# Kernel tuning notes

Hardware: AMD Instinct MI355X
Metric: run time of the kernel (lower is better)

Reference implementation:

```python
import jax, jax.numpy as jnp
import numpy as np

B, N, C, H = 8, 512, 64, 128
T, K = 10, 2                       # dilation threshold and skip divisor
TAUS = (0.25, 0.5, 0.75)
WTS = (0.25, 0.5, 0.25)
EPS_GIN = 0.0                      # (1 + eps) * x, eps buffer
AVG_DEG = 32.0


def setup_inputs() -> dict:
    key = jax.random.key(0)
    ks = jax.random.split(key, 6)
    x = jax.random.normal(ks[0], (B, N, C), jnp.float32)
    u = jax.random.uniform(ks[1], (B, N, N))
    a = u < (AVG_DEG / N)
    adj = jnp.maximum(a, jnp.swapaxes(a, 1, 2)).astype(jnp.float32)  # symmetric binary adjacency
    mask = jax.random.bernoulli(ks[2], 0.9, (B, N))
    W1 = jax.random.normal(ks[3], (C, H), jnp.float32) / np.float32(np.sqrt(C))
    b1 = jnp.zeros((H,), jnp.float32)
    W2 = jax.random.normal(ks[4], (H, C), jnp.float32) / np.float32(np.sqrt(H))
    b2 = jnp.zeros((C,), jnp.float32)
    return {"x": x, "adj": adj, "mask": mask, "W1": W1, "b1": b1, "W2": W2, "b2": b2}


def reference(x, adj, mask, W1, b1, W2, b2):
    Bc, Nc, Cc = x.shape
    eye = jnp.eye(Nc, dtype=bool)
    adj_ = jnp.where(eye, 1.0, adj)                 # add_loop=True: force self loops
    # ---- vectorized dilation (replaces the per-(b,n) python loop) ----
    neigh = (adj_ > 0) & (~eye)                     # neighbors excluding self [B,N,N]
    ni = neigh.astype(jnp.int32)
    rank = jnp.cumsum(ni, axis=-1) - ni             # exclusive rank of m among n's sorted neighbors
    nb = ni.sum(-1)                                 # [B,N] neighbor count (w/o self)
    skip = jnp.where(nb > T, (nb + K - 1) // K, 1)  # ceil(nb/k) if nb > T else 1 (linear mode, layer 1)
    skip = jnp.maximum(skip, 1)
    sk = skip[:, :, None]
    # remove relative indices skip-1, 2*skip-1, ... when skip > 1, only for masked-in nodes
    rem = neigh & (sk > 1) & ((rank % sk) == (sk - 1)) & mask[:, :, None]
    rem = rem | jnp.swapaxes(rem, 1, 2)             # symmetric removal
    adj_d = jnp.where(rem, 0.0, adj_)
    # ---- masked quantile aggregation over neighbors (== nanquantile) ----
    nd = adj_d > 0                                  # includes self loop -> at least 1 valid
    vals = jnp.where(nd[..., None], x[:, None, :, :], jnp.inf)  # [B,N,M,C]; invalid -> +inf
    s = jnp.sort(vals, axis=2)                      # valid values first, ascending
    nv = nd.sum(2)                                  # [B,N] valid count per node
    agg = jnp.zeros_like(x)
    for tau, w in zip(TAUS, WTS):                   # small fixed loop over quantiles
        pos = jnp.asarray(tau, x.dtype) * jnp.maximum(nv - 1, 0).astype(x.dtype)
        lo = jnp.floor(pos).astype(jnp.int32)
        hi = jnp.ceil(pos).astype(jnp.int32)
        frac = (pos - lo.astype(x.dtype))[..., None]
        idx_lo = jnp.broadcast_to(lo[:, :, None, None], (Bc, Nc, 1, Cc))
        idx_hi = jnp.broadcast_to(hi[:, :, None, None], (Bc, Nc, 1, Cc))
        v_lo = jnp.take_along_axis(s, idx_lo, axis=2)[:, :, 0, :]
        v_hi = jnp.take_along_axis(s, idx_hi, axis=2)[:, :, 0, :]
        agg = agg + jnp.asarray(w, x.dtype) * (v_lo + frac * (v_hi - v_lo))
    agg = jnp.where(nv[..., None] > 0, agg, 0.0)    # nan_to_num for empty rows
    out = (1.0 + EPS_GIN) * x + agg
    h = jax.nn.relu(out @ W1 + b1)                  # GIN MLP: Linear-ReLU-Linear
    y = h @ W2 + b2
    return y * mask[..., None].astype(y.dtype)
```

## Files before the change

### kernel.cpp

```cpp
#include <hip/hip_runtime.h>
#include <cstdint>

#define B_ 8
#define N_ 512
#define C_ 64
#define H_ 128
#define T_ 10
#define K_ 2
#define WPR 16
#define NVMAX 96
#define TT 8

__device__ inline uint32_t fkey(float v) {
    uint32_t bits = __float_as_uint(v);
    return (bits & 0x80000000u) ? ~bits : (bits | 0x80000000u);
}
__device__ inline float fdec(uint32_t key) {
    uint32_t ok = (key & 0xFFFFFF00u) | 0x80u;
    uint32_t bits = (ok & 0x80000000u) ? (ok ^ 0x80000000u) : ~ok;
    return __uint_as_float(bits);
}

__global__ __launch_bounds__(256) void pass1_rem(const float* __restrict__ adj,
                                                 const int* __restrict__ mask,
                                                 uint32_t* __restrict__ rembits) {
    int wid = threadIdx.x >> 6, lane = threadIdx.x & 63;
    int row = blockIdx.x * 4 + wid;
    int i = row & (N_ - 1);
    const float4* arow4 = (const float4*)(adj + (size_t)row * N_);
    float4 a0 = arow4[lane * 2];
    float4 a1 = arow4[lane * 2 + 1];
    float av[8] = {a0.x, a0.y, a0.z, a0.w, a1.x, a1.y, a1.z, a1.w};

    int flags = 0, cnt = 0;
    int jbase = lane * 8;
#pragma unroll
    for (int k = 0; k < 8; ++k) {
        int j = jbase + k;
        bool ng = (j != i) && (av[k] > 0.0f);
        flags |= ((int)ng) << k;
        cnt += (int)ng;
    }
    int inc = cnt;
#pragma unroll
    for (int d = 1; d < 64; d <<= 1) {
        int o = __shfl_up(inc, d, 64);
        if (lane >= d) inc += o;
    }
    int excl = inc - cnt;
    int nb = __shfl(inc, 63, 64);
    int skip = (nb > T_) ? ((nb + K_ - 1) / K_) : 1;
    if (skip < 1) skip = 1;
    int maski = mask[row];

    unsigned byteval = 0;
    if (skip > 1 && maski != 0) {
        int r = excl;
#pragma unroll
        for (int k = 0; k < 8; ++k) {
            if ((flags >> k) & 1) {
                if (r % skip == skip - 1) byteval |= 1u << k;
                ++r;
            }
        }
    }
    unsigned b0 = __shfl((int)byteval, (lane & 15) * 4 + 0, 64);
    unsigned b1 = __shfl((int)byteval, (lane & 15) * 4 + 1, 64);
    unsigned b2 = __shfl((int)byteval, (lane & 15) * 4 + 2, 64);
    unsigned b3 = __shfl((int)byteval, (lane & 15) * 4 + 3, 64);
    if (lane < WPR) {
        uint32_t w = b0 | (b1 << 8) | (b2 << 16) | (b3 << 24);
        rembits[(size_t)row * WPR + lane] = w;
    }
}

__global__ __launch_bounds__(256) void pass2_quant_mlp(
        const float* __restrict__ x, const float* __restrict__ adj,
        const int* __restrict__ mask, const uint32_t* __restrict__ rembits,
        const float* __restrict__ W1, const float* __restrict__ b1,
        const float* __restrict__ W2, const float* __restrict__ b2,
        float* __restrict__ out) {
    int row = blockIdx.x;
    int b = row >> 9, i = row & (N_ - 1);
    int tid = threadIdx.x;
    int lane = tid & 63;
    int q = tid >> 6;

    __shared__ unsigned short kept[NVMAX];
    __shared__ int s_cnt;
    __shared__ uint32_t keys[NVMAX * C_];
    __shared__ float selv[6][C_];
    __shared__ int s_rr[6];
    __shared__ float s_frac[3];
    __shared__ float out_node[C_];
    __shared__ float hbuf[H_];

    if (tid == 0) s_cnt = 0;
    __syncthreads();

    const float* arow = adj + (size_t)row * N_;
    const uint32_t* rrow = rembits + (size_t)row * WPR;
    const uint32_t* rbase = rembits + (size_t)(b * N_) * WPR;

    for (int jb = 0; jb < N_; jb += 256) {
        int j = jb + tid;
        bool keep;
        if (j == i) {
            keep = true;
        } else {
            keep = (arow[j] > 0.0f);
            if (keep) {
                unsigned rij = (rrow[j >> 5] >> (j & 31)) & 1u;
                unsigned rji = (rbase[(size_t)j * WPR + (i >> 5)] >> (i & 31)) & 1u;
                keep = ((rij | rji) == 0u);
            }
        }
        unsigned long long bal = __ballot(keep);
        int base = 0;
        if (lane == 0 && bal) base = atomicAdd(&s_cnt, __popcll(bal));
        base = __shfl(base, 0, 64);
        if (keep) {
            int pos = __popcll(bal & ((1ull << lane) - 1ull));
            int p = base + pos;
            if (p < NVMAX) kept[p] = (unsigned short)j;
        }
    }
    __syncthreads();
    int nv = s_cnt;
    if (nv > NVMAX) nv = NVMAX;

    const float* xb = x + (size_t)b * N_ * C_;

    for (int t = q; t < nv; t += 4) {
        float v = xb[(size_t)kept[t] * C_ + lane];
        keys[t * C_ + lane] = (fkey(v) & 0xFFFFFF00u) | (uint32_t)t;
    }

    if (tid == 0) {
        const float taus[3] = {0.25f, 0.5f, 0.75f};
        float nm1 = (float)((nv - 1 > 0) ? nv - 1 : 0);
        for (int qq = 0; qq < 3; ++qq) {
            float pos = taus[qq] * nm1;
            int lo = (int)floorf(pos);
            int hi = (int)ceilf(pos);
            s_rr[2 * qq] = lo; s_rr[2 * qq + 1] = hi;
            s_frac[qq] = pos - (float)lo;
        }
    }
    __syncthreads();

    int rr0 = s_rr[0], rr1 = s_rr[1], rr2 = s_rr[2],
        rr3 = s_rr[3], rr4 = s_rr[4], rr5 = s_rr[5];

    const uint32_t* kcol = keys + lane;

    for (int base = 0; base < nv; base += 32) {
        int tbase = base + q * TT;
        if (tbase >= nv) continue;
        uint32_t k[TT];
        int rs_a[TT], rs_b[TT];
#pragma unroll
        for (int m = 0; m < TT; ++m) {
            int t = tbase + m;
            k[m] = (t < nv) ? kcol[t * C_] : 0xFFFFFFFFu;
            rs_a[m] = 0; rs_b[m] = 0;
        }
        int u = 0;
#pragma unroll 2
        for (; u + 1 < nv; u += 2) {
            uint32_t w0 = kcol[u * C_];
            uint32_t w1 = kcol[(u + 1) * C_];
#pragma unroll
            for (int m = 0; m < TT; ++m) {
                rs_a[m] += (int)(w0 < k[m]);
                rs_b[m] += (int)(w1 < k[m]);
            }
        }
        if (u < nv) {
            uint32_t w0 = kcol[u * C_];
#pragma unroll
            for (int m = 0; m < TT; ++m) rs_a[m] += (int)(w0 < k[m]);
        }
#pragma unroll
        for (int m = 0; m < TT; ++m) {
            int rs = rs_a[m] + rs_b[m];
            bool h0 = rs == rr0, h1 = rs == rr1, h2 = rs == rr2;
            bool h3 = rs == rr3, h4 = rs == rr4, h5 = rs == rr5;
            if (h0 | h1 | h2 | h3 | h4 | h5) {
                float fv = fdec(k[m]);
                if (h0) selv[0][lane] = fv;
                if (h1) selv[1][lane] = fv;
                if (h2) selv[2][lane] = fv;
                if (h3) selv[3][lane] = fv;
                if (h4) selv[4][lane] = fv;
                if (h5) selv[5][lane] = fv;
            }
        }
    }
    __syncthreads();

    if (tid < C_) {
        float f0 = s_frac[0], f1 = s_frac[1], f2 = s_frac[2];
        float agg = 0.25f * (selv[0][tid] + f0 * (selv[1][tid] - selv[0][tid]));
        agg      += 0.5f  * (selv[2][tid] + f1 * (selv[3][tid] - selv[2][tid]));
        agg      += 0.25f * (selv[4][tid] + f2 * (selv[5][tid] - selv[4][tid]));
        out_node[tid] = xb[(size_t)i * C_ + tid] + agg;
    }
    __syncthreads();

    float maskf = (mask[row] != 0) ? 1.0f : 0.0f;
    if (tid < H_) {
        float acc = b1[tid];
        for (int c = 0; c < C_; ++c) acc += out_node[c] * W1[c * H_ + tid];
        hbuf[tid] = acc > 0.0f ? acc : 0.0f;
    }
    __syncthreads();
    if (tid < C_) {
        float acc = b2[tid];
        for (int k = 0; k < H_; ++k) acc += hbuf[k] * W2[k * C_ + tid];
        out[(size_t)row * C_ + tid] = acc * maskf;
    }
}

extern "C" void kernel_launch(void* const* d_in, const int* in_sizes, int n_in,
                              void* d_out, int out_size, void* d_ws, size_t ws_size,
                              hipStream_t stream) {
    const float* x   = (const float*)d_in[0];
    const float* adj = (const float*)d_in[1];
    const int*  mask = (const int*)d_in[2];
    const float* W1  = (const float*)d_in[3];
    const float* b1  = (const float*)d_in[4];
    const float* W2  = (const float*)d_in[5];
    const float* b2  = (const float*)d_in[6];
    float* out = (float*)d_out;

    uint32_t* rembits = (uint32_t*)d_ws;

    hipLaunchKernelGGL(pass1_rem, dim3(B_ * N_ / 4), dim3(256), 0, stream,
                       adj, mask, rembits);
    hipLaunchKernelGGL(pass2_quant_mlp, dim3(B_ * N_), dim3(256), 0, stream,
                       x, adj, mask, rembits, W1, b1, W2, b2, out);
}
```

Measured before the change: 165.2 us.

## Precompute keep bitmask in pass1 and transpose sort keys into uint4 columns

Pass1 now writes a per-row keep bitmask (adjacency plus self loop minus removed edges), so pass2 reads only bitmasks and no longer touches the dense float adjacency row. The rank-counting keys move to a transposed, padded uint4 layout, so each lane reads four keys per LDS access instead of one strided word. The padded stride of 25 is meant to avoid bank conflicts. Padding to a multiple of four with sentinel keys makes the count loop branch-free. The cost is that keep symmetry now depends on looking up the transposed bit in the other row.

```diff
diff --git a/kernel.cpp b/kernel.cpp
--- a/kernel.cpp
+++ b/kernel.cpp
@@ -10,6 +10,7 @@
 #define WPR 16
 #define NVMAX 96
 #define TT 8
+#define KS4 25
 
 __device__ inline uint32_t fkey(float v) {
     uint32_t bits = __float_as_uint(v);
@@ -21,9 +22,9 @@
     return __uint_as_float(bits);
 }
 
-__global__ __launch_bounds__(256) void pass1_rem(const float* __restrict__ adj,
-                                                 const int* __restrict__ mask,
-                                                 uint32_t* __restrict__ rembits) {
+__global__ __launch_bounds__(256) void pass1_keep(const float* __restrict__ adj,
+                                                  const int* __restrict__ mask,
+                                                  uint32_t* __restrict__ keepbits) {
     int wid = threadIdx.x >> 6, lane = threadIdx.x & 63;
     int row = blockIdx.x * 4 + wid;
     int i = row & (N_ - 1);
@@ -53,30 +54,34 @@
     if (skip < 1) skip = 1;
     int maski = mask[row];
 
-    unsigned byteval = 0;
+    unsigned remb = 0;
     if (skip > 1 && maski != 0) {
         int r = excl;
 #pragma unroll
         for (int k = 0; k < 8; ++k) {
             if ((flags >> k) & 1) {
-                if (r % skip == skip - 1) byteval |= 1u << k;
+                if (r % skip == skip - 1) remb |= 1u << k;
                 ++r;
             }
         }
     }
-    unsigned b0 = __shfl((int)byteval, (lane & 15) * 4 + 0, 64);
-    unsigned b1 = __shfl((int)byteval, (lane & 15) * 4 + 1, 64);
-    unsigned b2 = __shfl((int)byteval, (lane & 15) * 4 + 2, 64);
-    unsigned b3 = __shfl((int)byteval, (lane & 15) * 4 + 3, 64);
+    unsigned diagb = (i >= jbase && i < jbase + 8) ? (1u << (i - jbase)) : 0u;
+    unsigned keepb = (((unsigned)flags | diagb) & ~remb) & 0xFFu;
+
+    unsigned p0 = __shfl((int)keepb, (lane & 15) * 4 + 0, 64);
+    unsigned p1 = __shfl((int)keepb, (lane & 15) * 4 + 1, 64);
+    unsigned p2 = __shfl((int)keepb, (lane & 15) * 4 + 2, 64);
+    unsigned p3 = __shfl((int)keepb, (lane & 15) * 4 + 3, 64);
     if (lane < WPR) {
-        uint32_t w = b0 | (b1 << 8) | (b2 << 16) | (b3 << 24);
-        rembits[(size_t)row * WPR + lane] = w;
+        uint32_t w = (p0 & 0xFFu) | ((p1 & 0xFFu) << 8) |
+                     ((p2 & 0xFFu) << 16) | ((p3 & 0xFFu) << 24);
+        keepbits[(size_t)row * WPR + lane] = w;
     }
 }
 
 __global__ __launch_bounds__(256) void pass2_quant_mlp(
-        const float* __restrict__ x, const float* __restrict__ adj,
-        const int* __restrict__ mask, const uint32_t* __restrict__ rembits,
+        const float* __restrict__ x,
+        const int* __restrict__ mask, const uint32_t* __restrict__ keepbits,
         const float* __restrict__ W1, const float* __restrict__ b1,
         const float* __restrict__ W2, const float* __restrict__ b2,
         float* __restrict__ out) {
@@ -86,9 +91,9 @@
     int lane = tid & 63;
     int q = tid >> 6;
 
+    __shared__ uint4 keysT4[C_ * KS4];
     __shared__ unsigned short kept[NVMAX];
     __shared__ int s_cnt;
-    __shared__ uint32_t keys[NVMAX * C_];
     __shared__ float selv[6][C_];
     __shared__ int s_rr[6];
     __shared__ float s_frac[3];
@@ -98,22 +103,16 @@
     if (tid == 0) s_cnt = 0;
     __syncthreads();
 
-    const float* arow = adj + (size_t)row * N_;
-    const uint32_t* rrow = rembits + (size_t)row * WPR;
-    const uint32_t* rbase = rembits + (size_t)(b * N_) * WPR;
+    const uint32_t* wrow  = keepbits + (size_t)row * WPR;
+    const uint32_t* wbase = keepbits + (size_t)(b * N_) * WPR;
 
     for (int jb = 0; jb < N_; jb += 256) {
         int j = jb + tid;
-        bool keep;
-        if (j == i) {
-            keep = true;
-        } else {
-            keep = (arow[j] > 0.0f);
-            if (keep) {
-                unsigned rij = (rrow[j >> 5] >> (j & 31)) & 1u;
-                unsigned rji = (rbase[(size_t)j * WPR + (i >> 5)] >> (i & 31)) & 1u;
-                keep = ((rij | rji) == 0u);
-            }
+        uint32_t aw = wrow[j >> 5];
+        bool keep = (aw >> (j & 31)) & 1u;
+        if (keep && j != i) {
+            uint32_t tw = wbase[(size_t)j * WPR + (i >> 5)];
+            keep = (tw >> (i & 31)) & 1u;
         }
         unsigned long long bal = __ballot(keep);
         int base = 0;
@@ -128,12 +127,23 @@
     __syncthreads();
     int nv = s_cnt;
     if (nv > NVMAX) nv = NVMAX;
+    int nvp = (nv + 3) & ~3;
 
     const float* xb = x + (size_t)b * N_ * C_;
 
-    for (int t = q; t < nv; t += 4) {
-        float v = xb[(size_t)kept[t] * C_ + lane];
-        keys[t * C_ + lane] = (fkey(v) & 0xFFFFFF00u) | (uint32_t)t;
+    for (int t0 = q * 4; t0 < nvp; t0 += 16) {
+        uint32_t kk[4];
+#pragma unroll
+        for (int e = 0; e < 4; ++e) {
+            int t = t0 + e;
+            uint32_t kv = 0xFFFFFFFFu;
+            if (t < nv) {
+                float v = xb[(size_t)kept[t] * C_ + lane];
+                kv = (fkey(v) & 0xFFFFFF00u) | (uint32_t)t;
+            }
+            kk[e] = kv;
+        }
+        keysT4[lane * KS4 + (t0 >> 2)] = make_uint4(kk[0], kk[1], kk[2], kk[3]);
     }
 
     if (tid == 0) {
@@ -152,38 +162,35 @@
     int rr0 = s_rr[0], rr1 = s_rr[1], rr2 = s_rr[2],
         rr3 = s_rr[3], rr4 = s_rr[4], rr5 = s_rr[5];
 
-    const uint32_t* kcol = keys + lane;
-
-    for (int base = 0; base < nv; base += 32) {
+    const uint4* col = &keysT4[lane * KS4];
+    int iters = nvp >> 2;
+
+    for (int base = 0; base < nvp; base += 32) {
         int tbase = base + q * TT;
-        if (tbase >= nv) continue;
-        uint32_t k[TT];
-        int rs_a[TT], rs_b[TT];
+        if (tbase >= nvp) continue;
+        uint4 ka = col[(tbase >> 2)];
+        uint4 kb = col[(tbase >> 2) + 1];
+        uint32_t k[TT] = {ka.x, ka.y, ka.z, ka.w, kb.x, kb.y, kb.z, kb.w};
+        int ra[TT], rb[TT];
 #pragma unroll
         for (int m = 0; m < TT; ++m) {
-            int t = tbase + m;
-            k[m] = (t < nv) ? kcol[t * C_] : 0xFFFFFFFFu;
-            rs_a[m] = 0; rs_b[m] = 0;
-        }
-        int u = 0;
+            if (tbase + m >= nv) k[m] = 0xFFFFFFFFu;
+            ra[m] = 0; rb[m] = 0;
+        }
 #pragma unroll 2
-        for (; u + 1 < nv; u += 2) {
-            uint32_t w0 = kcol[u * C_];
-            uint32_t w1 = kcol[(u + 1) * C_];
+        for (int it = 0; it < iters; ++it) {
+            uint4 w = col[it];
 #pragma unroll
             for (int m = 0; m < TT; ++m) {
-                rs_a[m] += (int)(w0 < k[m]);
-                rs_b[m] += (int)(w1 < k[m]);
-            }
-        }
-        if (u < nv) {
-            uint32_t w0 = kcol[u * C_];
-#pragma unroll
-            for (int m = 0; m < TT; ++m) rs_a[m] += (int)(w0 < k[m]);
+                ra[m] += (int)(w.x < k[m]);
+                rb[m] += (int)(w.y < k[m]);
+                ra[m] += (int)(w.z < k[m]);
+                rb[m] += (int)(w.w < k[m]);
+            }
         }
 #pragma unroll
         for (int m = 0; m < TT; ++m) {
-            int rs = rs_a[m] + rs_b[m];
+            int rs = ra[m] + rb[m];
             bool h0 = rs == rr0, h1 = rs == rr1, h2 = rs == rr2;
             bool h3 = rs == rr3, h4 = rs == rr4, h5 = rs == rr5;
             if (h0 | h1 | h2 | h3 | h4 | h5) {
@@ -217,7 +224,7 @@
     __syncthreads();
     if (tid < C_) {
         float acc = b2[tid];
-        for (int k = 0; k < H_; ++k) acc += hbuf[k] * W2[k * C_ + tid];
+        for (int k2 = 0; k2 < H_; ++k2) acc += hbuf[k2] * W2[k2 * C_ + tid];
         out[(size_t)row * C_ + tid] = acc * maskf;
     }
 }
@@ -234,10 +241,10 @@
     const float* b2  = (const float*)d_in[6];
     float* out = (float*)d_out;
 
-    uint32_t* rembits = (uint32_t*)d_ws;
-
-    hipLaunchKernelGGL(pass1_rem, dim3(B_ * N_ / 4), dim3(256), 0, stream,
-                       adj, mask, rembits);
+    uint32_t* keepbits = (uint32_t*)d_ws;
+
+    hipLaunchKernelGGL(pass1_keep, dim3(B_ * N_ / 4), dim3(256), 0, stream,
+                       adj, mask, keepbits);
     hipLaunchKernelGGL(pass2_quant_mlp, dim3(B_ * N_), dim3(256), 0, stream,
-                       x, adj, mask, rembits, W1, b1, W2, b2, out);
-}
+                       x, mask, keepbits, W1, b1, W2, b2, out);
+}
```

Measured after the change: 171.0 us. +3.5%, slower.

## Precompute symmetric keep bitmask via bit-transpose pass; split MLP across threads

Applied to the files above, without the earlier changes.

Pass 1 now writes a keep bitmask (neighbors plus self, minus removed entries). A new per-batch kernel does 32x32 bit-matrix transposes in shared memory and ANDs each tile with its transpose, which makes the removal symmetric. Pass 2 then reads only its own 16-word bit row instead of the adjacency row and scattered transposed rembits, so it does not touch adj at all. The MLP stage is also split over all 256 threads with partial sums, and the per-row quantile index math moves into registers. The trade-off is an extra launch that runs only 8 blocks.

```diff
diff --git a/kernel.cpp b/kernel.cpp
--- a/kernel.cpp
+++ b/kernel.cpp
@@ -21,9 +21,23 @@
     return __uint_as_float(bits);
 }
 
-__global__ __launch_bounds__(256) void pass1_rem(const float* __restrict__ adj,
-                                                 const int* __restrict__ mask,
-                                                 uint32_t* __restrict__ rembits) {
+__device__ __forceinline__ uint32_t bittr32(uint32_t x, int kk) {
+    const int ss[5] = {16, 8, 4, 2, 1};
+    const uint32_t mm[5] = {0x0000FFFFu, 0x00FF00FFu, 0x0F0F0F0Fu,
+                            0x33333333u, 0x55555555u};
+#pragma unroll
+    for (int t = 0; t < 5; ++t) {
+        int s = ss[t]; uint32_t Ms = mm[t];
+        uint32_t y = (uint32_t)__shfl_xor((int)x, s, 64);
+        x = (kk & s) ? ((x & ~Ms) | ((y & ~Ms) >> s))
+                     : ((x & Ms)  | ((y & Ms)  << s));
+    }
+    return x;
+}
+
+__global__ __launch_bounds__(256) void pass1_keep(const float* __restrict__ adj,
+                                                  const int* __restrict__ mask,
+                                                  uint32_t* __restrict__ keepbits) {
     int wid = threadIdx.x >> 6, lane = threadIdx.x & 63;
     int row = blockIdx.x * 4 + wid;
     int i = row & (N_ - 1);
@@ -53,30 +67,63 @@
     if (skip < 1) skip = 1;
     int maski = mask[row];
 
-    unsigned byteval = 0;
+    unsigned remb = 0;
     if (skip > 1 && maski != 0) {
         int r = excl;
 #pragma unroll
         for (int k = 0; k < 8; ++k) {
             if ((flags >> k) & 1) {
-                if (r % skip == skip - 1) byteval |= 1u << k;
+                if (r % skip == skip - 1) remb |= 1u << k;
                 ++r;
             }
         }
     }
-    unsigned b0 = __shfl((int)byteval, (lane & 15) * 4 + 0, 64);
-    unsigned b1 = __shfl((int)byteval, (lane & 15) * 4 + 1, 64);
-    unsigned b2 = __shfl((int)byteval, (lane & 15) * 4 + 2, 64);
-    unsigned b3 = __shfl((int)byteval, (lane & 15) * 4 + 3, 64);
+    unsigned diagb = (i >= jbase && i < jbase + 8) ? (1u << (i - jbase)) : 0u;
+    unsigned keepb = (((unsigned)flags | diagb) & ~remb) & 0xFFu;
+
+    unsigned p0 = __shfl((int)keepb, (lane & 15) * 4 + 0, 64);
+    unsigned p1 = __shfl((int)keepb, (lane & 15) * 4 + 1, 64);
+    unsigned p2 = __shfl((int)keepb, (lane & 15) * 4 + 2, 64);
+    unsigned p3 = __shfl((int)keepb, (lane & 15) * 4 + 3, 64);
     if (lane < WPR) {
-        uint32_t w = b0 | (b1 << 8) | (b2 << 16) | (b3 << 24);
-        rembits[(size_t)row * WPR + lane] = w;
-    }
+        uint32_t w = (p0 & 0xFFu) | ((p1 & 0xFFu) << 8) |
+                     ((p2 & 0xFFu) << 16) | ((p3 & 0xFFu) << 24);
+        keepbits[(size_t)row * WPR + lane] = w;
+    }
+}
+
+__global__ __launch_bounds__(256) void pass1p5_transpose_and(uint32_t* __restrict__ kb) {
+    int bb = blockIdx.x;
+    int tid = threadIdx.x;
+    int g32 = tid >> 5;
+    int kk  = tid & 31;
+    __shared__ uint32_t w1p[N_ * 17];
+    uint32_t* g = kb + (size_t)bb * N_ * WPR;
+
+    for (int idx = tid; idx < N_ * WPR; idx += 256)
+        w1p[(idx >> 4) * 17 + (idx & 15)] = g[idx];
+    __syncthreads();
+
+    for (int unit = g32; unit < 136; unit += 8) {
+        int R = 0, u = unit;
+        while (u >= 16 - R) { u -= 16 - R; ++R; }
+        int G = R + u;
+        uint32_t A  = w1p[(32 * R + kk) * 17 + G];
+        uint32_t Bt = (R == G) ? A : w1p[(32 * G + kk) * 17 + R];
+        uint32_t At  = bittr32(A, kk);
+        uint32_t Btt = bittr32(Bt, kk);
+        w1p[(32 * R + kk) * 17 + G] = A & Btt;
+        if (R != G) w1p[(32 * G + kk) * 17 + R] = Bt & At;
+    }
+    __syncthreads();
+
+    for (int idx = tid; idx < N_ * WPR; idx += 256)
+        g[idx] = w1p[(idx >> 4) * 17 + (idx & 15)];
 }
 
 __global__ __launch_bounds__(256) void pass2_quant_mlp(
-        const float* __restrict__ x, const float* __restrict__ adj,
-        const int* __restrict__ mask, const uint32_t* __restrict__ rembits,
+        const float* __restrict__ x,
+        const int* __restrict__ mask, const uint32_t* __restrict__ keepbits,
         const float* __restrict__ W1, const float* __restrict__ b1,
         const float* __restrict__ W2, const float* __restrict__ b2,
         float* __restrict__ out) {
@@ -90,31 +137,19 @@
     __shared__ int s_cnt;
     __shared__ uint32_t keys[NVMAX * C_];
     __shared__ float selv[6][C_];
-    __shared__ int s_rr[6];
-    __shared__ float s_frac[3];
-    __shared__ float out_node[C_];
-    __shared__ float hbuf[H_];
+    float* mlp_buf = (float*)keys;
 
     if (tid == 0) s_cnt = 0;
     __syncthreads();
 
-    const float* arow = adj + (size_t)row * N_;
-    const uint32_t* rrow = rembits + (size_t)row * WPR;
-    const uint32_t* rbase = rembits + (size_t)(b * N_) * WPR;
-
+    const float* xb = x + (size_t)b * N_ * C_;
+    float xself = xb[(size_t)i * C_ + lane];
+    int mv = mask[row];
+
+    const uint32_t* krow = keepbits + (size_t)row * WPR;
     for (int jb = 0; jb < N_; jb += 256) {
         int j = jb + tid;
-        bool keep;
-        if (j == i) {
-            keep = true;
-        } else {
-            keep = (arow[j] > 0.0f);
-            if (keep) {
-                unsigned rij = (rrow[j >> 5] >> (j & 31)) & 1u;
-                unsigned rji = (rbase[(size_t)j * WPR + (i >> 5)] >> (i & 31)) & 1u;
-                keep = ((rij | rji) == 0u);
-            }
-        }
+        bool keep = (krow[j >> 5] >> (j & 31)) & 1u;
         unsigned long long bal = __ballot(keep);
         int base = 0;
         if (lane == 0 && bal) base = atomicAdd(&s_cnt, __popcll(bal));
@@ -129,28 +164,17 @@
     int nv = s_cnt;
     if (nv > NVMAX) nv = NVMAX;
 
-    const float* xb = x + (size_t)b * N_ * C_;
-
     for (int t = q; t < nv; t += 4) {
         float v = xb[(size_t)kept[t] * C_ + lane];
         keys[t * C_ + lane] = (fkey(v) & 0xFFFFFF00u) | (uint32_t)t;
     }
 
-    if (tid == 0) {
-        const float taus[3] = {0.25f, 0.5f, 0.75f};
-        float nm1 = (float)((nv - 1 > 0) ? nv - 1 : 0);
-        for (int qq = 0; qq < 3; ++qq) {
-            float pos = taus[qq] * nm1;
-            int lo = (int)floorf(pos);
-            int hi = (int)ceilf(pos);
-            s_rr[2 * qq] = lo; s_rr[2 * qq + 1] = hi;
-            s_frac[qq] = pos - (float)lo;
-        }
-    }
-    __syncthreads();
-
-    int rr0 = s_rr[0], rr1 = s_rr[1], rr2 = s_rr[2],
-        rr3 = s_rr[3], rr4 = s_rr[4], rr5 = s_rr[5];
+    float nm1 = (float)((nv - 1 > 0) ? nv - 1 : 0);
+    float p0 = 0.25f * nm1, p1 = 0.5f * nm1, p2 = 0.75f * nm1;
+    int rr0 = (int)floorf(p0), rr1 = (int)ceilf(p0);
+    int rr2 = (int)floorf(p1), rr3 = (int)ceilf(p1);
+    int rr4 = (int)floorf(p2), rr5 = (int)ceilf(p2);
+    __syncthreads();
 
     const uint32_t* kcol = keys + lane;
 
@@ -169,11 +193,11 @@
 #pragma unroll 2
         for (; u + 1 < nv; u += 2) {
             uint32_t w0 = kcol[u * C_];
-            uint32_t w1 = kcol[(u + 1) * C_];
+            uint32_t w1v = kcol[(u + 1) * C_];
 #pragma unroll
             for (int m = 0; m < TT; ++m) {
                 rs_a[m] += (int)(w0 < k[m]);
-                rs_b[m] += (int)(w1 < k[m]);
+                rs_b[m] += (int)(w1v < k[m]);
             }
         }
         if (u < nv) {
@@ -200,25 +224,47 @@
     __syncthreads();
 
     if (tid < C_) {
-        float f0 = s_frac[0], f1 = s_frac[1], f2 = s_frac[2];
+        float f0 = p0 - floorf(p0), f1 = p1 - floorf(p1), f2 = p2 - floorf(p2);
         float agg = 0.25f * (selv[0][tid] + f0 * (selv[1][tid] - selv[0][tid]));
         agg      += 0.5f  * (selv[2][tid] + f1 * (selv[3][tid] - selv[2][tid]));
         agg      += 0.25f * (selv[4][tid] + f2 * (selv[5][tid] - selv[4][tid]));
-        out_node[tid] = xb[(size_t)i * C_ + tid] + agg;
-    }
-    __syncthreads();
-
-    float maskf = (mask[row] != 0) ? 1.0f : 0.0f;
+        mlp_buf[tid] = xself + agg;
+    }
+    __syncthreads();
+
+    {
+        int hcol = tid & 127, chalf = tid >> 7;
+        float acc = 0.0f;
+#pragma unroll 4
+        for (int c = 0; c < 32; ++c) {
+            int c0 = chalf * 32 + c;
+            acc += mlp_buf[c0] * W1[c0 * H_ + hcol];
+        }
+        mlp_buf[192 + tid] = acc;
+    }
+    __syncthreads();
     if (tid < H_) {
-        float acc = b1[tid];
-        for (int c = 0; c < C_; ++c) acc += out_node[c] * W1[c * H_ + tid];
-        hbuf[tid] = acc > 0.0f ? acc : 0.0f;
+        float h = mlp_buf[192 + tid] + mlp_buf[192 + tid + 128] + b1[tid];
+        mlp_buf[64 + tid] = h > 0.0f ? h : 0.0f;
+    }
+    __syncthreads();
+
+    {
+        int ycol = tid & 63, kq = tid >> 6;
+        float acc = 0.0f;
+#pragma unroll 4
+        for (int kk = 0; kk < 32; ++kk) {
+            int k0 = kq * 32 + kk;
+            acc += mlp_buf[64 + k0] * W2[k0 * C_ + ycol];
+        }
+        mlp_buf[192 + tid] = acc;
     }
     __syncthreads();
     if (tid < C_) {
-        float acc = b2[tid];
-        for (int k = 0; k < H_; ++k) acc += hbuf[k] * W2[k * C_ + tid];
-        out[(size_t)row * C_ + tid] = acc * maskf;
+        float maskf = (mv != 0) ? 1.0f : 0.0f;
+        float y = b2[tid] + mlp_buf[192 + tid] + mlp_buf[192 + tid + 64]
+                + mlp_buf[192 + tid + 128] + mlp_buf[192 + tid + 192];
+        out[(size_t)row * C_ + tid] = y * maskf;
     }
 }
 
@@ -234,10 +280,12 @@
     const float* b2  = (const float*)d_in[6];
     float* out = (float*)d_out;
 
-    uint32_t* rembits = (uint32_t*)d_ws;
-
-    hipLaunchKernelGGL(pass1_rem, dim3(B_ * N_ / 4), dim3(256), 0, stream,
-                       adj, mask, rembits);
+    uint32_t* keepbits = (uint32_t*)d_ws;
+
+    hipLaunchKernelGGL(pass1_keep, dim3(B_ * N_ / 4), dim3(256), 0, stream,
+                       adj, mask, keepbits);
+    hipLaunchKernelGGL(pass1p5_transpose_and, dim3(B_), dim3(256), 0, stream,
+                       keepbits);
     hipLaunchKernelGGL(pass2_quant_mlp, dim3(B_ * N_), dim3(256), 0, stream,
-                       x, adj, mask, rembits, W1, b1, W2, b2, out);
-}
+                       x, mask, keepbits, W1, b1, W2, b2, out);
+}
```

New measurement: 177.1 us. 7.2% more time.
